# Optimization experiments

Measured on AMD Instinct MI355X. Metric: run time of the kernel, lower is better.

## Reference

```python
import jax, jax.numpy as jnp
import numpy as np

B, L, D = 1, 1024, 128
EPS = 1e-5


def setup_inputs() -> dict:
    key = jax.random.key(0)
    ks = jax.random.split(key, 10)
    s = 1.0 / np.sqrt(D)
    return {
        "x": jax.random.normal(ks[0], (B, L, D), dtype=jnp.float32),
        "mask": jax.random.randint(ks[1], (B, L, L), 0, 2, dtype=jnp.int32),
        # JCrossOutProduct.l : Linear(D, D)
        "Wl": jax.random.uniform(ks[2], (D, D), jnp.float32, -s, s),
        "bl": jax.random.uniform(ks[3], (D,), jnp.float32, -s, s),
        # JCrossOutProduct.lo : Linear(D, D)
        "Wlo": jax.random.uniform(ks[4], (D, D), jnp.float32, -s, s),
        "blo": jax.random.uniform(ks[5], (D,), jnp.float32, -s, s),
        # JResCOPAttn.l : Linear(D, D)
        "Wl2": jax.random.uniform(ks[6], (D, D), jnp.float32, -s, s),
        "bl2": jax.random.uniform(ks[7], (D,), jnp.float32, -s, s),
        # LayerNorm(D)
        "gamma": jnp.ones((D,), jnp.float32),
        "beta": jnp.zeros((D,), jnp.float32),
    }


def reference(x, mask, Wl, bl, Wlo, blo, Wl2, bl2, gamma, beta):
    # a = self.cop.l(x) : [B, L, D]
    a = x @ Wl.T + bl
    # outer product kept per-channel: [B, L, L, D]
    outer = jnp.einsum('blc,bmc->blmc', a, a)
    # self.cop.lo over last dim: [B, L, L, D]
    tm = outer @ Wlo.T + blo
    # masked_fill(mask.unsqueeze(-1) == 0, 0.0)
    tm = tm * (mask[..., None] != 0).astype(tm.dtype)
    # tx = self.l(x)
    tx = x @ Wl2.T + bl2
    # per-channel attention-like contraction: out[b,c,d] = sum_a tm[b,c,a,d] * tx[b,a,d]
    y = x + jnp.einsum('bcad,bad->bcd', tm, tx)
    # shadow (eval): Dropout=identity, activator 'none'=identity, LayerNorm(D)
    mu = jnp.mean(y, axis=-1, keepdims=True)
    var = jnp.mean(jnp.square(y - mu), axis=-1, keepdims=True)
    return (y - mu) * jax.lax.rsqrt(var + EPS) * gamma + beta
```

## Files before the change

kernel.cpp:

```cpp
#include <hip/hip_runtime.h>
#include <hip/hip_fp16.h>


typedef _Float16 f16x8 __attribute__((ext_vector_type(8)));
typedef float    f32x4 __attribute__((ext_vector_type(4)));
typedef unsigned int       u32;
typedef unsigned long long u64;

#define LL   1024
#define DD   128
#define MCH  32
#define TPAD 34
#define EPSV 1e-5f

__global__ __launch_bounds__(256) void prep_kernel(
    const float* __restrict__ x,  const float* __restrict__ Wl,
    const float* __restrict__ bl, const float* __restrict__ Wlo,
    const float* __restrict__ Wl2,const float* __restrict__ bl2,
    _Float16* __restrict__ a_h, float* __restrict__ tx_out,
    _Float16* __restrict__ wh)
{
    __shared__ float xs[16*128];
    __shared__ float wsh[64*129];
    const int t  = threadIdx.x;
    const int bx = blockIdx.x;
    const int by = blockIdx.y;
    const int l0 = by*16;

    #pragma unroll
    for (int i = 0; i < 8; ++i) { int f = i*256 + t; xs[f] = x[l0*DD + f]; }
    const float* Wsrc = ((bx < 2) ? Wl : Wl2) + (bx & 1)*64*DD;
    #pragma unroll
    for (int i = 0; i < 32; ++i) {
        int f = i*256 + t; int r = f >> 7, k = f & 127;
        wsh[r*129 + k] = Wsrc[f];
    }
    __syncthreads();

    const int col  = t & 63;
    const int lsub = t >> 6;
    const float4* X4 = (const float4*)xs;
    float acc0 = 0.f, acc1 = 0.f, acc2 = 0.f, acc3 = 0.f;
    #pragma unroll
    for (int k4 = 0; k4 < 32; ++k4) {
        const float* wp = wsh + col*129 + k4*4;
        float4 wv = {wp[0], wp[1], wp[2], wp[3]};
        float4 x0 = X4[(lsub*4+0)*32 + k4];
        float4 x1 = X4[(lsub*4+1)*32 + k4];
        float4 x2 = X4[(lsub*4+2)*32 + k4];
        float4 x3 = X4[(lsub*4+3)*32 + k4];
        acc0 += wv.x*x0.x + wv.y*x0.y + wv.z*x0.z + wv.w*x0.w;
        acc1 += wv.x*x1.x + wv.y*x1.y + wv.z*x1.z + wv.w*x1.w;
        acc2 += wv.x*x2.x + wv.y*x2.y + wv.z*x2.z + wv.w*x2.w;
        acc3 += wv.x*x3.x + wv.y*x3.y + wv.z*x3.z + wv.w*x3.w;
    }
    const int colg = (bx & 1)*64 + col;
    const float bv = ((bx < 2) ? bl : bl2)[colg];
    if (bx < 2) {
        a_h[(l0+lsub*4+0)*DD + colg] = (_Float16)(acc0 + bv);
        a_h[(l0+lsub*4+1)*DD + colg] = (_Float16)(acc1 + bv);
        a_h[(l0+lsub*4+2)*DD + colg] = (_Float16)(acc2 + bv);
        a_h[(l0+lsub*4+3)*DD + colg] = (_Float16)(acc3 + bv);
    } else {
        tx_out[(l0+lsub*4+0)*DD + colg] = acc0 + bv;
        tx_out[(l0+lsub*4+1)*DD + colg] = acc1 + bv;
        tx_out[(l0+lsub*4+2)*DD + colg] = acc2 + bv;
        tx_out[(l0+lsub*4+3)*DD + colg] = acc3 + bv;
    }

    const int gid = (by*4 + bx)*256 + t;
    if (gid < DD*DD) wh[gid] = (_Float16)Wlo[gid];
}

#define COMPUTE(MI, AM, TV)                                                   \
  do {                                                                        \
    f16x8 ah_[4];                                                             \
    _Pragma("unroll")                                                         \
    for (int k_ = 0; k_ < 4; ++k_) ah_[k_] = al[k_] * (AM)[k_];               \
    f32x4 c_[4];                                                              \
    _Pragma("unroll")                                                         \
    for (int nf_ = 0; nf_ < 4; ++nf_)                                         \
      c_[nf_] = f32x4{blov[nf_], blov[nf_], blov[nf_], blov[nf_]};            \
    _Pragma("unroll")                                                         \
    for (int k_ = 0; k_ < 4; ++k_) {                                          \
      c_[0] = __builtin_amdgcn_mfma_f32_16x16x32_f16(ah_[k_], bh[0][k_], c_[0],0,0,0); \
      c_[1] = __builtin_amdgcn_mfma_f32_16x16x32_f16(ah_[k_], bh[1][k_], c_[1],0,0,0); \
      c_[2] = __builtin_amdgcn_mfma_f32_16x16x32_f16(ah_[k_], bh[2][k_], c_[2],0,0,0); \
      c_[3] = __builtin_amdgcn_mfma_f32_16x16x32_f16(ah_[k_], bh[3][k_], c_[3],0,0,0); \
    }                                                                         \
    _Pragma("unroll")                                                         \
    for (int r_ = 0; r_ < 4; ++r_) {                                          \
      const bool on_ = ((wmb[r_] >> (MI)) & 1u) != 0;                         \
      _Pragma("unroll")                                                       \
      for (int nf_ = 0; nf_ < 4; ++nf_)                                       \
        y[nf_][r_] = fmaf(on_ ? (TV)[nf_] : 0.0f, c_[nf_][r_], y[nf_][r_]);   \
    }                                                                         \
  } while (0)

__global__ __launch_bounds__(256, 2) void heavy_kernel(
    const _Float16* __restrict__ a_h, const float* __restrict__ tx,
    const _Float16* __restrict__ wh,  const int* __restrict__ mask,
    const float* __restrict__ blo,    _Float16* __restrict__ part)
{
    __shared__ __align__(16) _Float16 ash[MCH*DD];
    __shared__ __align__(4)  _Float16 txt[DD*TPAD];
    __shared__ u32 mbits[32];
    const int t     = threadIdx.x;
    const int lane  = t & 63, w = t >> 6;
    const int chunk = blockIdx.x;
    const int ltile = blockIdx.y;
    const int l0 = ltile*32, m0 = chunk*MCH;

    {
        const float4* s4 = (const float4*)(a_h + m0*DD);
        float4* d4 = (float4*)ash;
        #pragma unroll
        for (int i = 0; i < 2; ++i) d4[i*256 + t] = s4[i*256 + t];
    }
    {
        #pragma unroll
        for (int i = 0; i < 4; ++i) {
            int idx = i*256 + t;
            int m = idx >> 5, dg = idx & 31;
            float4 v = *(const float4*)(tx + (m0+m)*DD + dg*4);
            txt[(dg*4+0)*TPAD + m] = (_Float16)v.x;
            txt[(dg*4+1)*TPAD + m] = (_Float16)v.y;
            txt[(dg*4+2)*TPAD + m] = (_Float16)v.z;
            txt[(dg*4+3)*TPAD + m] = (_Float16)v.w;
        }
    }
    {
        #pragma unroll
        for (int i = 0; i < 4; ++i) {
            int idx = i*256 + t;
            int row = idx >> 5, mcol = idx & 31;
            u64 b = __ballot(mask[(l0 + row)*LL + m0 + mcol] != 0);
            if (lane == 0)  mbits[row]     = (u32)b;
            if (lane == 32) mbits[row]     = (u32)(b >> 32);
        }
    }
    __syncthreads();

    const int grp = lane >> 4, ln = lane & 15;
    const int wl = w >> 1, wd = w & 1;
    const int lbase = l0 + wl*16;
    const int dbase = wd*64;

    f16x8 bh[4][4];
    #pragma unroll
    for (int nf = 0; nf < 4; ++nf)
        #pragma unroll
        for (int k = 0; k < 4; ++k)
            bh[nf][k] = *(const f16x8*)(wh + (dbase + nf*16 + ln)*DD + k*32 + grp*8);

    f16x8 al[4];
    #pragma unroll
    for (int k = 0; k < 4; ++k)
        al[k] = *(const f16x8*)(a_h + (lbase + ln)*DD + k*32 + grp*8);

    float blov[4];
    #pragma unroll
    for (int nf = 0; nf < 4; ++nf) blov[nf] = blo[dbase + nf*16 + ln];

    const int lrow0 = wl*16 + grp*4;
    u32 wmb[4];
    #pragma unroll
    for (int r = 0; r < 4; ++r) wmb[r] = mbits[lrow0 + r];

    f32x4 y[4] = {{0,0,0,0},{0,0,0,0},{0,0,0,0},{0,0,0,0}};

    f16x8 amA[4], amB[4];
    float tvA[4], tvB[4];
    #pragma unroll
    for (int k = 0; k < 4; ++k)
        amA[k] = *(const f16x8*)(ash + 0*DD + k*32 + grp*8);

    for (int ms = 0; ms < 30; ms += 2) {
        #pragma unroll
        for (int k = 0; k < 4; ++k)
            amB[k] = *(const f16x8*)(ash + (ms+1)*DD + k*32 + grp*8);
        #pragma unroll
        for (int nf = 0; nf < 4; ++nf) {
            float2 f2 = __half22float2(
                *(const __half2*)(txt + (dbase + nf*16 + ln)*TPAD + ms));
            tvA[nf] = f2.x; tvB[nf] = f2.y;
        }
        COMPUTE(ms, amA, tvA);
        #pragma unroll
        for (int k = 0; k < 4; ++k)
            amA[k] = *(const f16x8*)(ash + (ms+2)*DD + k*32 + grp*8);
        COMPUTE(ms+1, amB, tvB);
    }
    {
        #pragma unroll
        for (int k = 0; k < 4; ++k)
            amB[k] = *(const f16x8*)(ash + 31*DD + k*32 + grp*8);
        #pragma unroll
        for (int nf = 0; nf < 4; ++nf) {
            float2 f2 = __half22float2(
                *(const __half2*)(txt + (dbase + nf*16 + ln)*TPAD + 30));
            tvA[nf] = f2.x; tvB[nf] = f2.y;
        }
        COMPUTE(30, amA, tvA);
        COMPUTE(31, amB, tvB);
    }

    _Float16* dst = part + (size_t)chunk*(LL*DD);
    const int mrow0 = lbase + grp*4;
    #pragma unroll
    for (int nf = 0; nf < 4; ++nf)
        #pragma unroll
        for (int r = 0; r < 4; ++r)
            dst[(mrow0 + r)*DD + dbase + nf*16 + ln] = (_Float16)y[nf][r];
}

__global__ __launch_bounds__(128) void finish_kernel(
    const float* __restrict__ x, const _Float16* __restrict__ part,
    const float* __restrict__ gamma, const float* __restrict__ beta,
    float* __restrict__ out)
{
    const int l = blockIdx.x, t = threadIdx.x;
    float v = x[l*DD + t];
    #pragma unroll
    for (int ch = 0; ch < 32; ++ch)
        v += (float)part[((size_t)ch*LL + l)*DD + t];

    float s = v, s2 = v*v;
    #pragma unroll
    for (int o = 32; o > 0; o >>= 1) {
        s  += __shfl_xor(s, o);
        s2 += __shfl_xor(s2, o);
    }
    __shared__ float red[4];
    if ((t & 63) == 0) { red[(t>>6)*2+0] = s; red[(t>>6)*2+1] = s2; }
    __syncthreads();
    const float S  = red[0] + red[2];
    const float S2 = red[1] + red[3];
    const float mu  = S * (1.0f/128.0f);
    const float var = S2 * (1.0f/128.0f) - mu*mu;
    const float inv = rsqrtf(var + EPSV);
    out[l*DD + t] = (v - mu)*inv*gamma[t] + beta[t];
}

extern "C" void kernel_launch(void* const* d_in, const int* in_sizes, int n_in,
                              void* d_out, int out_size, void* d_ws, size_t ws_size,
                              hipStream_t stream)
{
    (void)in_sizes; (void)n_in; (void)out_size; (void)ws_size;
    const float* x     = (const float*)d_in[0];
    const int*   mask  = (const int*)  d_in[1];
    const float* Wl    = (const float*)d_in[2];
    const float* bl    = (const float*)d_in[3];
    const float* Wlo   = (const float*)d_in[4];
    const float* blo   = (const float*)d_in[5];
    const float* Wl2   = (const float*)d_in[6];
    const float* bl2   = (const float*)d_in[7];
    const float* gamma = (const float*)d_in[8];
    const float* beta  = (const float*)d_in[9];
    float* out = (float*)d_out;

    char* ws = (char*)d_ws;
    _Float16* a_h  = (_Float16*)(ws);
    float*    tx_b = (float*)   (ws + (256u<<10));
    _Float16* wh   = (_Float16*)(ws + (768u<<10));
    _Float16* part = (_Float16*)(ws + (1024u<<10));

    prep_kernel  <<<dim3(4,64),  256, 0, stream>>>(x, Wl, bl, Wlo, Wl2, bl2,
                                                   a_h, tx_b, wh);
    heavy_kernel <<<dim3(32,32), 256, 0, stream>>>(a_h, tx_b, wh, mask, blo, part);
    finish_kernel<<<1024, 128, 0, stream>>>(x, part, gamma, beta, out);
}
```

Before: 117.4 us.

## Split MFMA K dimension across warps and double the m-chunk per block

```diff
diff --git a/kernel.cpp b/kernel.cpp
--- a/kernel.cpp
+++ b/kernel.cpp
@@ -9,8 +9,8 @@
 
 #define LL   1024
 #define DD   128
-#define MCH  32
-#define TPAD 34
+#define MCH  64
+#define TPAD 66
 #define EPSV 1e-5f
 
 __global__ __launch_bounds__(256) void prep_kernel(
@@ -72,39 +72,57 @@
     if (gid < DD*DD) wh[gid] = (_Float16)Wlo[gid];
 }
 
-#define COMPUTE(MI, AM, TV)                                                   \
+#define COMPUTE(MI, AM, TV, WM)                                               \
   do {                                                                        \
-    f16x8 ah_[4];                                                             \
-    _Pragma("unroll")                                                         \
-    for (int k_ = 0; k_ < 4; ++k_) ah_[k_] = al[k_] * (AM)[k_];               \
+    f16x8 ah_[2];                                                             \
+    ah_[0] = al[0] * (AM)[0];                                                 \
+    ah_[1] = al[1] * (AM)[1];                                                 \
     f32x4 c_[4];                                                              \
     _Pragma("unroll")                                                         \
     for (int nf_ = 0; nf_ < 4; ++nf_)                                         \
       c_[nf_] = f32x4{blov[nf_], blov[nf_], blov[nf_], blov[nf_]};            \
     _Pragma("unroll")                                                         \
-    for (int k_ = 0; k_ < 4; ++k_) {                                          \
-      c_[0] = __builtin_amdgcn_mfma_f32_16x16x32_f16(ah_[k_], bh[0][k_], c_[0],0,0,0); \
-      c_[1] = __builtin_amdgcn_mfma_f32_16x16x32_f16(ah_[k_], bh[1][k_], c_[1],0,0,0); \
-      c_[2] = __builtin_amdgcn_mfma_f32_16x16x32_f16(ah_[k_], bh[2][k_], c_[2],0,0,0); \
-      c_[3] = __builtin_amdgcn_mfma_f32_16x16x32_f16(ah_[k_], bh[3][k_], c_[3],0,0,0); \
+    for (int kf_ = 0; kf_ < 2; ++kf_) {                                       \
+      c_[0] = __builtin_amdgcn_mfma_f32_16x16x32_f16(ah_[kf_], bh[0][kf_], c_[0],0,0,0); \
+      c_[1] = __builtin_amdgcn_mfma_f32_16x16x32_f16(ah_[kf_], bh[1][kf_], c_[1],0,0,0); \
+      c_[2] = __builtin_amdgcn_mfma_f32_16x16x32_f16(ah_[kf_], bh[2][kf_], c_[2],0,0,0); \
+      c_[3] = __builtin_amdgcn_mfma_f32_16x16x32_f16(ah_[kf_], bh[3][kf_], c_[3],0,0,0); \
     }                                                                         \
     _Pragma("unroll")                                                         \
     for (int r_ = 0; r_ < 4; ++r_) {                                          \
-      const bool on_ = ((wmb[r_] >> (MI)) & 1u) != 0;                         \
+      const bool on_ = (((WM)[r_] >> (MI)) & 1u) != 0;                        \
       _Pragma("unroll")                                                       \
       for (int nf_ = 0; nf_ < 4; ++nf_)                                       \
         y[nf_][r_] = fmaf(on_ ? (TV)[nf_] : 0.0f, c_[nf_][r_], y[nf_][r_]);   \
     }                                                                         \
   } while (0)
 
-__global__ __launch_bounds__(256, 2) void heavy_kernel(
+#define HALF_LOOP(WM, MOFF)                                                   \
+  for (int ms = 0; ms < 32; ms += 2) {                                        \
+    f16x8 am0[2], am1[2];                                                     \
+    am0[0] = *(const f16x8*)(ash + (MOFF + ms)*DD     + kbase + 0*32 + grp*8);\
+    am0[1] = *(const f16x8*)(ash + (MOFF + ms)*DD     + kbase + 1*32 + grp*8);\
+    am1[0] = *(const f16x8*)(ash + (MOFF + ms + 1)*DD + kbase + 0*32 + grp*8);\
+    am1[1] = *(const f16x8*)(ash + (MOFF + ms + 1)*DD + kbase + 1*32 + grp*8);\
+    float tvA[4], tvB[4];                                                     \
+    _Pragma("unroll")                                                         \
+    for (int nf = 0; nf < 4; ++nf) {                                          \
+      float2 f2 = __half22float2(                                             \
+          *(const __half2*)(txt + (dbase + nf*16 + ln)*TPAD + MOFF + ms));    \
+      tvA[nf] = f2.x; tvB[nf] = f2.y;                                         \
+    }                                                                         \
+    COMPUTE(ms,     am0, tvA, WM);                                            \
+    COMPUTE(ms + 1, am1, tvB, WM);                                            \
+  }
+
+__global__ __launch_bounds__(512, 4) void heavy_kernel(
     const _Float16* __restrict__ a_h, const float* __restrict__ tx,
     const _Float16* __restrict__ wh,  const int* __restrict__ mask,
     const float* __restrict__ blo,    _Float16* __restrict__ part)
 {
     __shared__ __align__(16) _Float16 ash[MCH*DD];
     __shared__ __align__(4)  _Float16 txt[DD*TPAD];
-    __shared__ u32 mbits[32];
+    __shared__ u64 mbits[32];
     const int t     = threadIdx.x;
     const int lane  = t & 63, w = t >> 6;
     const int chunk = blockIdx.x;
@@ -115,12 +133,12 @@
         const float4* s4 = (const float4*)(a_h + m0*DD);
         float4* d4 = (float4*)ash;
         #pragma unroll
-        for (int i = 0; i < 2; ++i) d4[i*256 + t] = s4[i*256 + t];
+        for (int i = 0; i < 2; ++i) d4[i*512 + t] = s4[i*512 + t];
     }
     {
         #pragma unroll
         for (int i = 0; i < 4; ++i) {
-            int idx = i*256 + t;
+            int idx = i*512 + t;
             int m = idx >> 5, dg = idx & 31;
             float4 v = *(const float4*)(tx + (m0+m)*DD + dg*4);
             txt[(dg*4+0)*TPAD + m] = (_Float16)v.x;
@@ -132,80 +150,56 @@
     {
         #pragma unroll
         for (int i = 0; i < 4; ++i) {
-            int idx = i*256 + t;
-            int row = idx >> 5, mcol = idx & 31;
+            int idx = i*512 + t;
+            int row = idx >> 6, mcol = idx & 63;
             u64 b = __ballot(mask[(l0 + row)*LL + m0 + mcol] != 0);
-            if (lane == 0)  mbits[row]     = (u32)b;
-            if (lane == 32) mbits[row]     = (u32)(b >> 32);
+            if ((t & 63) == 0) mbits[row] = b;
         }
     }
     __syncthreads();
 
     const int grp = lane >> 4, ln = lane & 15;
-    const int wl = w >> 1, wd = w & 1;
+    const int wl = w >> 2, wd = (w >> 1) & 1, kh = w & 1;
     const int lbase = l0 + wl*16;
     const int dbase = wd*64;
-
-    f16x8 bh[4][4];
+    const int kbase = kh*64;
+
+    f16x8 bh[4][2];
     #pragma unroll
     for (int nf = 0; nf < 4; ++nf)
         #pragma unroll
-        for (int k = 0; k < 4; ++k)
-            bh[nf][k] = *(const f16x8*)(wh + (dbase + nf*16 + ln)*DD + k*32 + grp*8);
-
-    f16x8 al[4];
-    #pragma unroll
-    for (int k = 0; k < 4; ++k)
-        al[k] = *(const f16x8*)(a_h + (lbase + ln)*DD + k*32 + grp*8);
+        for (int kf = 0; kf < 2; ++kf)
+            bh[nf][kf] = *(const f16x8*)(wh + (dbase + nf*16 + ln)*DD
+                                            + kbase + kf*32 + grp*8);
+
+    f16x8 al[2];
+    #pragma unroll
+    for (int kf = 0; kf < 2; ++kf)
+        al[kf] = *(const f16x8*)(a_h + (lbase + ln)*DD + kbase + kf*32 + grp*8);
 
     float blov[4];
-    #pragma unroll
-    for (int nf = 0; nf < 4; ++nf) blov[nf] = blo[dbase + nf*16 + ln];
+    if (kh == 0) {
+        #pragma unroll
+        for (int nf = 0; nf < 4; ++nf) blov[nf] = blo[dbase + nf*16 + ln];
+    } else {
+        #pragma unroll
+        for (int nf = 0; nf < 4; ++nf) blov[nf] = 0.0f;
+    }
 
     const int lrow0 = wl*16 + grp*4;
-    u32 wmb[4];
-    #pragma unroll
-    for (int r = 0; r < 4; ++r) wmb[r] = mbits[lrow0 + r];
+    u32 wmbL[4], wmbH[4];
+    #pragma unroll
+    for (int r = 0; r < 4; ++r) {
+        u64 b = mbits[lrow0 + r];
+        wmbL[r] = (u32)b; wmbH[r] = (u32)(b >> 32);
+    }
 
     f32x4 y[4] = {{0,0,0,0},{0,0,0,0},{0,0,0,0},{0,0,0,0}};
 
-    f16x8 amA[4], amB[4];
-    float tvA[4], tvB[4];
-    #pragma unroll
-    for (int k = 0; k < 4; ++k)
-        amA[k] = *(const f16x8*)(ash + 0*DD + k*32 + grp*8);
-
-    for (int ms = 0; ms < 30; ms += 2) {
-        #pragma unroll
-        for (int k = 0; k < 4; ++k)
-            amB[k] = *(const f16x8*)(ash + (ms+1)*DD + k*32 + grp*8);
-        #pragma unroll
-        for (int nf = 0; nf < 4; ++nf) {
-            float2 f2 = __half22float2(
-                *(const __half2*)(txt + (dbase + nf*16 + ln)*TPAD + ms));
-            tvA[nf] = f2.x; tvB[nf] = f2.y;
-        }
-        COMPUTE(ms, amA, tvA);
-        #pragma unroll
-        for (int k = 0; k < 4; ++k)
-            amA[k] = *(const f16x8*)(ash + (ms+2)*DD + k*32 + grp*8);
-        COMPUTE(ms+1, amB, tvB);
-    }
-    {
-        #pragma unroll
-        for (int k = 0; k < 4; ++k)
-            amB[k] = *(const f16x8*)(ash + 31*DD + k*32 + grp*8);
-        #pragma unroll
-        for (int nf = 0; nf < 4; ++nf) {
-            float2 f2 = __half22float2(
-                *(const __half2*)(txt + (dbase + nf*16 + ln)*TPAD + 30));
-            tvA[nf] = f2.x; tvB[nf] = f2.y;
-        }
-        COMPUTE(30, amA, tvA);
-        COMPUTE(31, amB, tvB);
-    }
-
-    _Float16* dst = part + (size_t)chunk*(LL*DD);
+    HALF_LOOP(wmbL, 0);
+    HALF_LOOP(wmbH, 32);
+
+    _Float16* dst = part + (size_t)(chunk*2 + kh)*(LL*DD);
     const int mrow0 = lbase + grp*4;
     #pragma unroll
     for (int nf = 0; nf < 4; ++nf)
@@ -267,6 +261,6 @@
 
     prep_kernel  <<<dim3(4,64),  256, 0, stream>>>(x, Wl, bl, Wlo, Wl2, bl2,
                                                    a_h, tx_b, wh);
-    heavy_kernel <<<dim3(32,32), 256, 0, stream>>>(a_h, tx_b, wh, mask, blo, part);
+    heavy_kernel <<<dim3(16,32), 512, 0, stream>>>(a_h, tx_b, wh, mask, blo, part);
     finish_kernel<<<1024, 128, 0, stream>>>(x, part, gamma, beta, out);
 }
```

New measurement: 137.0 us. +16.7%, slower.
